# Performance work log

Hardware: AMD Instinct MI355X
Metric: run time of the kernel (lower is better)

Reference implementation:

```python
import jax, jax.numpy as jnp
import numpy as np

N = 50000          # nodes
E_RAND = 800000    # random edges
E = E_RAND + N     # + self loops -> 850000
F_IN = 256         # nembed
F_HID = 64         # nhid
H = 8              # nheads
NCLASS = 40
ALPHA = 0.2        # leakyrelu slope


def setup_inputs() -> dict:
    key = jax.random.key(0)
    ks = jax.random.split(key, 8)
    x = jax.random.normal(ks[0], (N, F_IN), dtype=jnp.float32)
    # random edges + self loops (guarantees every row-sum > 0, like adj + I)
    er = jax.random.randint(ks[1], (2, E_RAND), 0, N, dtype=jnp.int32)
    loops = jnp.tile(jnp.arange(N, dtype=jnp.int32)[None, :], (2, 1))
    edge_index = jnp.concatenate([er, loops], axis=1)  # [2, E]
    # per-head attention params (xavier-ish scale)
    W = jax.random.normal(ks[2], (H, F_IN, F_HID), dtype=jnp.float32) * (1.0 / np.sqrt(F_IN))
    a = jax.random.normal(ks[3], (H, 2 * F_HID), dtype=jnp.float32) * 0.1
    Wo = jax.random.normal(ks[4], (H * F_HID, F_HID), dtype=jnp.float32) * (1.0 / np.sqrt(H * F_HID))
    ao = jax.random.normal(ks[5], (2 * F_HID,), dtype=jnp.float32) * 0.1
    mlp_w = jax.random.normal(ks[6], (NCLASS, F_HID), dtype=jnp.float32) * 0.05
    mlp_b = jnp.zeros((NCLASS,), dtype=jnp.float32)
    return {"x": x, "edge_index": edge_index, "W": W, "a": a,
            "Wo": Wo, "ao": ao, "mlp_w": mlp_w, "mlp_b": mlp_b}


def _leaky(v):
    return jnp.where(v > 0, v, ALPHA * v)


def _spgat_layer(x, W, a, src, dst, n):
    """pyGAT SpGraphAttentionLayer (eval mode, dropout = identity).
    out[i] = sum_{e: src=i} exp(-leakyrelu(a.[h_src;h_dst])) * h[dst] / rowsum_i
    """
    h = x @ W                         # [N, D]
    D = W.shape[1]
    s_src = h @ a[:D]                 # [N]
    s_dst = h @ a[D:]                 # [N]
    # per-edge unnormalized attention (note the -exp(leaky) of original sp impl)
    e = jnp.exp(-_leaky(s_src[src] + s_dst[dst]))          # [E]
    rowsum = jax.ops.segment_sum(e, src, num_segments=n)   # [N]
    num = jax.ops.segment_sum(e[:, None] * h[dst], src, num_segments=n)  # [N, D]
    return num / rowsum[:, None]


def reference(x, edge_index, W, a, Wo, ao, mlp_w, mlp_b):
    src, dst = edge_index[0], edge_index[1]
    # multi-head attention, concat=True -> elu inside each head
    heads = [jax.nn.elu(_spgat_layer(x, W[i], a[i], src, dst, N)) for i in range(H)]
    xc = jnp.concatenate(heads, axis=1)                     # [N, H*F_HID]
    # dropout (eval) = identity
    xo = jax.nn.elu(_spgat_layer(xc, Wo, ao, src, dst, N))  # [N, F_HID]
    return xo @ mlp_w.T + mlp_b                             # [N, NCLASS]
```

## Files before the change

### kernel.cpp

```cpp
#include <hip/hip_runtime.h>

#define NN 50000
#define HH 8
#define ALPHA 0.2f
#define NPAD 50048

typedef short short8 __attribute__((ext_vector_type(8)));
typedef float f32x4 __attribute__((ext_vector_type(4)));

__device__ __forceinline__ float elu_f(float x) {
  return x > 0.f ? x : __expf(x) - 1.f;
}

__device__ __forceinline__ unsigned short f2bf(float f) {
  unsigned int u = __float_as_uint(f);
  unsigned int r = (u + 0x7fffu + ((u >> 16) & 1u)) >> 16;
  return (unsigned short)r;
}

__global__ void cvt_all_kernel(const float* __restrict__ x, unsigned short* __restrict__ xb,
                               const float* __restrict__ W, unsigned short* __restrict__ Wt,
                               const float* __restrict__ Wo, unsigned short* __restrict__ Wot,
                               int n4x) {
  int tid = blockIdx.x * 256 + threadIdx.x;
  if (tid < n4x) {
    float4 v = ((const float4*)x)[tid];
    ushort4 o;
    o.x = f2bf(v.x); o.y = f2bf(v.y); o.z = f2bf(v.z); o.w = f2bf(v.w);
    ((ushort4*)xb)[tid] = o;
    return;
  }
  int t1 = tid - n4x;
  if (t1 < HH * 256 * 64) {
    int h = t1 / (256 * 64);
    int rem = t1 - h * 256 * 64;
    int k = rem >> 6, c = rem & 63;
    Wt[((size_t)h * 64 + c) * 256 + k] = f2bf(W[t1]);
    return;
  }
  int t2 = t1 - HH * 256 * 64;
  if (t2 < 512 * 64) {
    int k = t2 >> 6, c = t2 & 63;
    Wot[(size_t)c * 512 + k] = f2bf(Wo[t2]);
  }
}

__global__ void hist_kernel(const int* __restrict__ src, int* __restrict__ cnt, int E) {
  int e = blockIdx.x * blockDim.x + threadIdx.x;
  if (e < E) atomicAdd(&cnt[src[e]], 1);
}

__global__ __launch_bounds__(1024) void scan_blocks_kernel(const int* __restrict__ cnt,
    int* __restrict__ tmp, int* __restrict__ bsum, int n) {
  __shared__ int sh[1024];
  int i = blockIdx.x * 1024 + threadIdx.x;
  int v = (i < n) ? cnt[i] : 0;
  sh[threadIdx.x] = v;
  __syncthreads();
  for (int off = 1; off < 1024; off <<= 1) {
    int t = (threadIdx.x >= off) ? sh[threadIdx.x - off] : 0;
    __syncthreads();
    sh[threadIdx.x] += t;
    __syncthreads();
  }
  if (i < n) tmp[i] = sh[threadIdx.x] - v;
  if (threadIdx.x == 1023) bsum[blockIdx.x] = sh[1023];
}

__global__ __launch_bounds__(64) void scan_top_kernel(const int* __restrict__ bsum,
    int* __restrict__ boffs, int nb) {
  int L = threadIdx.x;
  int v = (L < nb) ? bsum[L] : 0;
  int incl = v;
#pragma unroll
  for (int off = 1; off < 64; off <<= 1) {
    int t = __shfl_up(incl, off, 64);
    if (L >= off) incl += t;
  }
  if (L < nb) boffs[L] = incl - v;
}

__global__ __launch_bounds__(1024) void scan_apply_kernel(const int* __restrict__ tmp,
    const int* __restrict__ boffs, int* __restrict__ row_ptr, int* __restrict__ nxt,
    int n, int E) {
  int i = blockIdx.x * 1024 + threadIdx.x;
  if (i < n) {
    int s = tmp[i] + boffs[blockIdx.x];
    row_ptr[i] = s;
    nxt[i] = s;
  }
  if (i == 0) row_ptr[n] = E;
}

__global__ void scatter_kernel(const int* __restrict__ src, const int* __restrict__ dst,
                               int* __restrict__ nxt, int* __restrict__ col, int E) {
  int e = blockIdx.x * blockDim.x + threadIdx.x;
  if (e < E) {
    int p = atomicAdd(&nxt[src[e]], 1);
    col[p] = dst[e];
  }
}

__global__ __launch_bounds__(256) void mfma_gemm1_kernel(
    const unsigned short* __restrict__ A, const unsigned short* __restrict__ Bt,
    const float* __restrict__ Aatt, unsigned short* __restrict__ Cout,
    float* __restrict__ ss, float* __restrict__ sd, int N) {
  __shared__ unsigned short Bs[64][264];
  int w = threadIdx.x >> 6, L = threadIdx.x & 63;
  int quad = L >> 4, l16 = L & 15;
  int m0 = blockIdx.x * 64;
  int myrow = m0 + w * 16 + l16;

  const unsigned short* Ar = A + (size_t)myrow * 256 + quad * 8;
  short8 areg[8];
#pragma unroll
  for (int ks = 0; ks < 8; ++ks) areg[ks] = *(const short8*)(Ar + ks * 32);

  for (int y = 0; y < HH; ++y) {
    __syncthreads();
    {
      const unsigned short* Bsrc = Bt + (size_t)y * 64 * 256;
      for (int c = threadIdx.x; c < 2048; c += 256) {
        int n = c >> 5;
        int kq = (c & 31) << 3;
        *(uint4*)&Bs[n][kq] = *(const uint4*)(Bsrc + (size_t)n * 256 + kq);
      }
    }
    __syncthreads();

    f32x4 acc[4];
#pragma unroll
    for (int nt = 0; nt < 4; ++nt) acc[nt] = (f32x4)(0.f);
#pragma unroll
    for (int ks = 0; ks < 8; ++ks) {
#pragma unroll
      for (int nt = 0; nt < 4; ++nt) {
        short8 b = *(const short8*)&Bs[l16 + 16 * nt][ks * 32 + quad * 8];
        acc[nt] = __builtin_amdgcn_mfma_f32_16x16x32_bf16(areg[ks], b, acc[nt], 0, 0, 0);
      }
    }

    float as[4], ad[4];
#pragma unroll
    for (int nt = 0; nt < 4; ++nt) {
      as[nt] = Aatt[y * 128 + l16 + 16 * nt];
      ad[nt] = Aatt[y * 128 + 64 + l16 + 16 * nt];
    }
#pragma unroll
    for (int reg = 0; reg < 4; ++reg) {
      float p = 0.f, q = 0.f;
#pragma unroll
      for (int nt = 0; nt < 4; ++nt) {
        p += acc[nt][reg] * as[nt];
        q += acc[nt][reg] * ad[nt];
      }
#pragma unroll
      for (int off = 1; off < 16; off <<= 1) {
        p += __shfl_xor(p, off, 64);
        q += __shfl_xor(q, off, 64);
      }
      int row = m0 + w * 16 + quad * 4 + reg;
      if (l16 == 0 && row < N) {
        ss[(size_t)row * 8 + y] = p;
        sd[(size_t)row * 8 + y] = q;
      }
    }
#pragma unroll
    for (int reg = 0; reg < 4; ++reg) {
      int row = m0 + w * 16 + quad * 4 + reg;
      if (row < N) {
#pragma unroll
        for (int nt = 0; nt < 4; ++nt)
          Cout[(size_t)row * 512 + y * 64 + l16 + 16 * nt] = f2bf(acc[nt][reg]);
      }
    }
  }
}

__global__ __launch_bounds__(256) void mfma_gemm2_kernel(
    const unsigned short* __restrict__ A, const unsigned short* __restrict__ Bt,
    const float* __restrict__ Aatt, unsigned short* __restrict__ Cout,
    float* __restrict__ ss, float* __restrict__ sd, int N) {
  __shared__ unsigned short Bs[64][520];
  {
    for (int c = threadIdx.x; c < 4096; c += 256) {
      int n = c >> 6;
      int kq = (c & 63) << 3;
      *(uint4*)&Bs[n][kq] = *(const uint4*)(Bt + (size_t)n * 512 + kq);
    }
  }
  __syncthreads();

  int w = threadIdx.x >> 6, L = threadIdx.x & 63;
  int quad = L >> 4, l16 = L & 15;
  int m0 = blockIdx.x * 64;
  int myrow = m0 + w * 16 + l16;
  const unsigned short* Ar = A + (size_t)myrow * 512 + quad * 8;

  f32x4 acc[4];
#pragma unroll
  for (int nt = 0; nt < 4; ++nt) acc[nt] = (f32x4)(0.f);

  short8 a_cur = *(const short8*)(Ar);
  for (int k0 = 0; k0 < 512; k0 += 32) {
    short8 a_nxt;
    if (k0 + 32 < 512) a_nxt = *(const short8*)(Ar + k0 + 32);
#pragma unroll
    for (int nt = 0; nt < 4; ++nt) {
      short8 b = *(const short8*)&Bs[l16 + 16 * nt][k0 + quad * 8];
      acc[nt] = __builtin_amdgcn_mfma_f32_16x16x32_bf16(a_cur, b, acc[nt], 0, 0, 0);
    }
    a_cur = a_nxt;
  }

  float as[4], ad[4];
#pragma unroll
  for (int nt = 0; nt < 4; ++nt) {
    as[nt] = Aatt[l16 + 16 * nt];
    ad[nt] = Aatt[64 + l16 + 16 * nt];
  }
#pragma unroll
  for (int reg = 0; reg < 4; ++reg) {
    float p = 0.f, q = 0.f;
#pragma unroll
    for (int nt = 0; nt < 4; ++nt) {
      p += acc[nt][reg] * as[nt];
      q += acc[nt][reg] * ad[nt];
    }
#pragma unroll
    for (int off = 1; off < 16; off <<= 1) {
      p += __shfl_xor(p, off, 64);
      q += __shfl_xor(q, off, 64);
    }
    int row = m0 + w * 16 + quad * 4 + reg;
    if (l16 == 0 && row < N) { ss[row] = p; sd[row] = q; }
  }
#pragma unroll
  for (int reg = 0; reg < 4; ++reg) {
    int row = m0 + w * 16 + quad * 4 + reg;
    if (row < N) {
#pragma unroll
      for (int nt = 0; nt < 4; ++nt)
        Cout[(size_t)row * 64 + l16 + 16 * nt] = f2bf(acc[nt][reg]);
    }
  }
}

__global__ __launch_bounds__(256) void agg1_kernel(const unsigned short* __restrict__ table,
    const float* __restrict__ ss, const float* __restrict__ sd,
    const int* __restrict__ row_ptr, const int* __restrict__ col,
    unsigned short* __restrict__ xc, int N) {
  int wid = threadIdx.x >> 6, L = threadIdx.x & 63;
  int n = blockIdx.x * 4 + wid;
  if (n >= N) return;
  int h = L >> 3;
  int b = L & 7;
  int srcsel = h << 3;
  float ssn = ss[n * 8 + h];
  int k0 = row_ptr[n], deg = row_ptr[n + 1] - k0;
  float acc[8];
#pragma unroll
  for (int t = 0; t < 8; ++t) acc[t] = 0.f;
  float rs = 0.f;

  for (int c0 = 0; c0 < deg; c0 += 64) {
    int j = c0 + L;
    int d_l = (j < deg) ? col[k0 + j] : 0;
    int m = min(64, deg - c0);
    for (int g = 0; g < m; g += 8) {
      int eoff = g + b;
      int de = __shfl(d_l, eoff, 64);
      float s = ssn + sd[(size_t)de * 8 + h];
      float e = __expf(-fmaxf(s, ALPHA * s));
      if (eoff >= m) e = 0.f;
      rs += e;
      int gm = min(8, m - g);
      uint4 rv[8];
#pragma unroll
      for (int t = 0; t < 8; ++t) {
        if (t < gm) {
          int dg = __builtin_amdgcn_readlane(d_l, g + t);
          rv[t] = *((const uint4*)(table + (size_t)dg * 512) + L);
        }
      }
#pragma unroll
      for (int t = 0; t < 8; ++t) {
        if (t < gm) {
          float ew = __shfl(e, srcsel + t, 64);
          const unsigned int* up = (const unsigned int*)&rv[t];
#pragma unroll
          for (int v = 0; v < 4; ++v) {
            acc[2 * v]     += ew * __uint_as_float(up[v] << 16);
            acc[2 * v + 1] += ew * __uint_as_float(up[v] & 0xffff0000u);
          }
        }
      }
    }
  }
  rs += __shfl_xor(rs, 1, 64);
  rs += __shfl_xor(rs, 2, 64);
  rs += __shfl_xor(rs, 4, 64);
  float inv = 1.f / rs;
  short8 pk;
#pragma unroll
  for (int t = 0; t < 8; ++t) pk[t] = (short)f2bf(elu_f(acc[t] * inv));
  *(short8*)(xc + (size_t)n * 512 + L * 8) = pk;
}

__global__ __launch_bounds__(256) void agg2_kernel(const unsigned short* __restrict__ table,
    const float* __restrict__ ss, const float* __restrict__ sd,
    const int* __restrict__ row_ptr, const int* __restrict__ col,
    float* __restrict__ xo, int N) {
  int wid = threadIdx.x >> 6, L = threadIdx.x & 63;
  int n = blockIdx.x * 4 + wid;
  if (n >= N) return;
  float ssn = ss[n];
  int k0 = row_ptr[n], deg = row_ptr[n + 1] - k0;
  float acc = 0.f, rs = 0.f;
  const char* base = (const char*)table;

  for (int c0 = 0; c0 < deg; c0 += 64) {
    int j = c0 + L;
    int d_l = 0;
    float e_l = 0.f;
    if (j < deg) {
      d_l = col[k0 + j];
      float s = ssn + sd[d_l];
      e_l = __expf(-fmaxf(s, ALPHA * s));
    }
    rs += e_l;
    int m = min(64, deg - c0);
    int off_l = d_l << 7;
    for (int g = 0; g < m; g += 8) {
      int gm = min(8, m - g);
      unsigned hv[8];
#pragma unroll
      for (int t = 0; t < 8; ++t) {
        if (t < gm) {
          int so = __builtin_amdgcn_readlane(off_l, g + t);
          hv[t] = *(const unsigned short*)(base + so + L * 2);
        }
      }
#pragma unroll
      for (int t = 0; t < 8; ++t) {
        if (t < gm) {
          float ew = __uint_as_float(
              (unsigned)__builtin_amdgcn_readlane(__float_as_uint(e_l), g + t));
          acc += ew * __uint_as_float(hv[t] << 16);
        }
      }
    }
  }
#pragma unroll
  for (int off = 1; off < 64; off <<= 1) rs += __shfl_xor(rs, off, 64);
  xo[(size_t)n * 64 + L] = elu_f(acc / rs);
}

__global__ __launch_bounds__(256) void final_kernel(const float* __restrict__ xo,
    const float* __restrict__ mlp_w, const float* __restrict__ mlp_b,
    float* __restrict__ out, int total) {
  __shared__ float wsh[40 * 65];
  __shared__ float bsh[40];
  for (int i = threadIdx.x; i < 40 * 64; i += 256) wsh[(i >> 6) * 65 + (i & 63)] = mlp_w[i];
  if (threadIdx.x < 40) bsh[threadIdx.x] = mlp_b[threadIdx.x];
  __syncthreads();
  int idx = blockIdx.x * 256 + threadIdx.x;
  if (idx >= total) return;
  int n = idx / 40, c = idx - n * 40;
  const float* xr = xo + (size_t)n * 64;
  const float* wr = wsh + c * 65;
  float acc = bsh[c];
#pragma unroll
  for (int j = 0; j < 64; ++j) acc += xr[j] * wr[j];
  out[idx] = acc;
}

extern "C" void kernel_launch(void* const* d_in, const int* in_sizes, int n_in,
                              void* d_out, int out_size, void* d_ws, size_t ws_size,
                              hipStream_t stream) {
  (void)n_in; (void)out_size; (void)ws_size;
  const float* x  = (const float*)d_in[0];
  const int*   ei = (const int*)d_in[1];
  const float* W  = (const float*)d_in[2];
  const float* a  = (const float*)d_in[3];
  const float* Wo = (const float*)d_in[4];
  const float* ao = (const float*)d_in[5];
  const float* mw = (const float*)d_in[6];
  const float* mb = (const float*)d_in[7];
  float* out = (float*)d_out;

  const int N = NN;
  const int E = in_sizes[1] / 2;
  const int* src = ei;
  const int* dst = ei + E;

  char* ws = (char*)d_ws;
  size_t off = 0;
  auto alloc = [&](size_t bytes) {
    char* p = ws + off;
    off = (off + bytes + 255) & ~(size_t)255;
    return p;
  };
  unsigned short* xb  = (unsigned short*)alloc((size_t)NPAD * 256 * 2);
  unsigned short* Wt  = (unsigned short*)alloc((size_t)HH * 64 * 256 * 2);
  unsigned short* Wot = (unsigned short*)alloc((size_t)64 * 512 * 2);
  unsigned short* h1b = (unsigned short*)alloc((size_t)N * 512 * 2);
  float* ss1     = (float*)alloc((size_t)N * 8 * 4);
  float* sd1     = (float*)alloc((size_t)N * 8 * 4);
  unsigned short* xc = (unsigned short*)alloc((size_t)NPAD * 512 * 2);
  unsigned short* h2b = (unsigned short*)alloc((size_t)N * 64 * 2);
  float* ss2     = (float*)alloc((size_t)N * 4);
  float* sd2     = (float*)alloc((size_t)N * 4);
  float* xo      = (float*)alloc((size_t)N * 64 * 4);
  int*   row_ptr = (int*)  alloc((size_t)(N + 1) * 4);
  int*   nxt     = (int*)  alloc((size_t)N * 4);
  int*   cnt     = (int*)  alloc((size_t)N * 4);
  int*   tmp     = (int*)  alloc((size_t)N * 4);
  int*   bsum    = (int*)  alloc(64 * 4);
  int*   boffs   = (int*)  alloc(64 * 4);
  int*   colv    = (int*)  alloc((size_t)E * 4);

  int eb = (E + 255) / 256;
  int nb1024 = (N + 1023) / 1024;
  int n4x = N * 256 / 4;
  int cvt_total = n4x + HH * 256 * 64 + 512 * 64;

  hipLaunchKernelGGL(cvt_all_kernel, dim3((cvt_total + 255) / 256), dim3(256), 0, stream,
                     x, xb, W, Wt, Wo, Wot, n4x);

  hipMemsetAsync(cnt, 0, (size_t)N * 4, stream);
  hipLaunchKernelGGL(hist_kernel, dim3(eb), dim3(256), 0, stream, src, cnt, E);
  hipLaunchKernelGGL(scan_blocks_kernel, dim3(nb1024), dim3(1024), 0, stream, cnt, tmp, bsum, N);
  hipLaunchKernelGGL(scan_top_kernel, dim3(1), dim3(64), 0, stream, bsum, boffs, nb1024);
  hipLaunchKernelGGL(scan_apply_kernel, dim3(nb1024), dim3(1024), 0, stream, tmp, boffs, row_ptr, nxt, N, E);
  hipLaunchKernelGGL(scatter_kernel, dim3(eb), dim3(256), 0, stream, src, dst, nxt, colv, E);

  hipLaunchKernelGGL(mfma_gemm1_kernel, dim3(NPAD / 64), dim3(256), 0, stream,
                     xb, Wt, a, h1b, ss1, sd1, N);
  hipLaunchKernelGGL(agg1_kernel, dim3((N + 3) / 4), dim3(256), 0, stream,
                     h1b, ss1, sd1, row_ptr, colv, xc, N);

  hipLaunchKernelGGL(mfma_gemm2_kernel, dim3(NPAD / 64), dim3(256), 0, stream,
                     xc, Wot, ao, h2b, ss2, sd2, N);
  hipLaunchKernelGGL(agg2_kernel, dim3((N + 3) / 4), dim3(256), 0, stream,
                     h2b, ss2, sd2, row_ptr, colv, xo, N);

  hipLaunchKernelGGL(final_kernel, dim3((N * 40 + 255) / 256), dim3(256), 0, stream,
                     xo, mw, mb, out, N * 40);
}
```

Baseline: 457.2 us.

## Fuse x bf16 conversion into GEMM1, fuse final MLP into agg2, dst-sort CSR

Drops the separate fp32-to-bf16 pass over x and converts rows on load inside the first MFMA GEMM. Fuses the output MLP into the second aggregation kernel through shared memory, so the xo intermediate is never written or reread. Rebuilds the CSR by first bucketing edges by destination, then scattering by source, so each row's column list comes out roughly sorted by dst and neighbour gathers are more local. The cost is extra histogram, scan and scatter work plus an eid buffer.

Measured after the change: 525.7 us. 15.0% more time.

```diff
diff --git a/kernel.cpp b/kernel.cpp
--- a/kernel.cpp
+++ b/kernel.cpp
@@ -18,43 +18,38 @@
   return (unsigned short)r;
 }
 
-__global__ void cvt_all_kernel(const float* __restrict__ x, unsigned short* __restrict__ xb,
-                               const float* __restrict__ W, unsigned short* __restrict__ Wt,
-                               const float* __restrict__ Wo, unsigned short* __restrict__ Wot,
-                               int n4x) {
+__global__ void cvt_w_kernel(const float* __restrict__ W, unsigned short* __restrict__ Wt,
+                             const float* __restrict__ Wo, unsigned short* __restrict__ Wot) {
   int tid = blockIdx.x * 256 + threadIdx.x;
-  if (tid < n4x) {
-    float4 v = ((const float4*)x)[tid];
-    ushort4 o;
-    o.x = f2bf(v.x); o.y = f2bf(v.y); o.z = f2bf(v.z); o.w = f2bf(v.w);
-    ((ushort4*)xb)[tid] = o;
+  if (tid < HH * 256 * 64) {
+    int h = tid / (256 * 64);
+    int rem = tid - h * 256 * 64;
+    int k = rem >> 6, c = rem & 63;
+    Wt[((size_t)h * 64 + c) * 256 + k] = f2bf(W[tid]);
     return;
   }
-  int t1 = tid - n4x;
-  if (t1 < HH * 256 * 64) {
-    int h = t1 / (256 * 64);
-    int rem = t1 - h * 256 * 64;
-    int k = rem >> 6, c = rem & 63;
-    Wt[((size_t)h * 64 + c) * 256 + k] = f2bf(W[t1]);
-    return;
-  }
-  int t2 = t1 - HH * 256 * 64;
+  int t2 = tid - HH * 256 * 64;
   if (t2 < 512 * 64) {
     int k = t2 >> 6, c = t2 & 63;
     Wot[(size_t)c * 512 + k] = f2bf(Wo[t2]);
   }
 }
 
-__global__ void hist_kernel(const int* __restrict__ src, int* __restrict__ cnt, int E) {
+__global__ void hist_both_kernel(const int* __restrict__ src, const int* __restrict__ dst,
+                                 int* __restrict__ cnt2, int N, int E) {
   int e = blockIdx.x * blockDim.x + threadIdx.x;
-  if (e < E) atomicAdd(&cnt[src[e]], 1);
-}
-
-__global__ __launch_bounds__(1024) void scan_blocks_kernel(const int* __restrict__ cnt,
-    int* __restrict__ tmp, int* __restrict__ bsum, int n) {
+  if (e < E) {
+    atomicAdd(&cnt2[src[e]], 1);
+    atomicAdd(&cnt2[N + dst[e]], 1);
+  }
+}
+
+__global__ __launch_bounds__(1024) void scan_blocks2_kernel(const int* __restrict__ cnt2,
+    int* __restrict__ tmp2, int* __restrict__ bsum2, int n) {
   __shared__ int sh[1024];
+  int y = blockIdx.y;
   int i = blockIdx.x * 1024 + threadIdx.x;
-  int v = (i < n) ? cnt[i] : 0;
+  int v = (i < n) ? cnt2[(size_t)y * n + i] : 0;
   sh[threadIdx.x] = v;
   __syncthreads();
   for (int off = 1; off < 1024; off <<= 1) {
@@ -63,46 +58,58 @@
     sh[threadIdx.x] += t;
     __syncthreads();
   }
-  if (i < n) tmp[i] = sh[threadIdx.x] - v;
-  if (threadIdx.x == 1023) bsum[blockIdx.x] = sh[1023];
-}
-
-__global__ __launch_bounds__(64) void scan_top_kernel(const int* __restrict__ bsum,
-    int* __restrict__ boffs, int nb) {
-  int L = threadIdx.x;
-  int v = (L < nb) ? bsum[L] : 0;
+  if (i < n) tmp2[(size_t)y * n + i] = sh[threadIdx.x] - v;
+  if (threadIdx.x == 1023) bsum2[y * 64 + blockIdx.x] = sh[1023];
+}
+
+__global__ __launch_bounds__(128) void scan_top2_kernel(const int* __restrict__ bsum2,
+    int* __restrict__ boffs2, int nb) {
+  int y = threadIdx.x >> 6, L = threadIdx.x & 63;
+  int v = (L < nb) ? bsum2[y * 64 + L] : 0;
   int incl = v;
 #pragma unroll
   for (int off = 1; off < 64; off <<= 1) {
     int t = __shfl_up(incl, off, 64);
     if (L >= off) incl += t;
   }
-  if (L < nb) boffs[L] = incl - v;
-}
-
-__global__ __launch_bounds__(1024) void scan_apply_kernel(const int* __restrict__ tmp,
-    const int* __restrict__ boffs, int* __restrict__ row_ptr, int* __restrict__ nxt,
-    int n, int E) {
+  if (L < nb) boffs2[y * 64 + L] = incl - v;
+}
+
+__global__ __launch_bounds__(1024) void scan_apply2_kernel(const int* __restrict__ tmp2,
+    const int* __restrict__ boffs2, int* __restrict__ row_ptr, int* __restrict__ nxt,
+    int* __restrict__ nxtd, int n, int E) {
+  int y = blockIdx.y;
   int i = blockIdx.x * 1024 + threadIdx.x;
   if (i < n) {
-    int s = tmp[i] + boffs[blockIdx.x];
-    row_ptr[i] = s;
-    nxt[i] = s;
-  }
-  if (i == 0) row_ptr[n] = E;
-}
-
-__global__ void scatter_kernel(const int* __restrict__ src, const int* __restrict__ dst,
-                               int* __restrict__ nxt, int* __restrict__ col, int E) {
+    int s = tmp2[(size_t)y * n + i] + boffs2[y * 64 + blockIdx.x];
+    if (y == 0) { row_ptr[i] = s; nxt[i] = s; }
+    else nxtd[i] = s;
+  }
+  if (i == 0 && y == 0) row_ptr[n] = E;
+}
+
+__global__ void scatter_d_kernel(const int* __restrict__ dst, int* __restrict__ nxtd,
+                                 int* __restrict__ eid, int E) {
   int e = blockIdx.x * blockDim.x + threadIdx.x;
   if (e < E) {
+    int p = atomicAdd(&nxtd[dst[e]], 1);
+    eid[p] = e;
+  }
+}
+
+__global__ void scatter_s_kernel(const int* __restrict__ src, const int* __restrict__ dst,
+                                 const int* __restrict__ eid, int* __restrict__ nxt,
+                                 int* __restrict__ col, int E) {
+  int k = blockIdx.x * blockDim.x + threadIdx.x;
+  if (k < E) {
+    int e = eid[k];
     int p = atomicAdd(&nxt[src[e]], 1);
     col[p] = dst[e];
   }
 }
 
 __global__ __launch_bounds__(256) void mfma_gemm1_kernel(
-    const unsigned short* __restrict__ A, const unsigned short* __restrict__ Bt,
+    const float* __restrict__ X, const unsigned short* __restrict__ Bt,
     const float* __restrict__ Aatt, unsigned short* __restrict__ Cout,
     float* __restrict__ ss, float* __restrict__ sd, int N) {
   __shared__ unsigned short Bs[64][264];
@@ -110,11 +117,19 @@
   int quad = L >> 4, l16 = L & 15;
   int m0 = blockIdx.x * 64;
   int myrow = m0 + w * 16 + l16;
-
-  const unsigned short* Ar = A + (size_t)myrow * 256 + quad * 8;
+  int rowc = min(myrow, N - 1);
+
+  const float* Ar = X + (size_t)rowc * 256 + quad * 8;
   short8 areg[8];
 #pragma unroll
-  for (int ks = 0; ks < 8; ++ks) areg[ks] = *(const short8*)(Ar + ks * 32);
+  for (int ks = 0; ks < 8; ++ks) {
+    float4 a0 = *(const float4*)(Ar + ks * 32);
+    float4 a1 = *(const float4*)(Ar + ks * 32 + 4);
+    areg[ks][0] = (short)f2bf(a0.x); areg[ks][1] = (short)f2bf(a0.y);
+    areg[ks][2] = (short)f2bf(a0.z); areg[ks][3] = (short)f2bf(a0.w);
+    areg[ks][4] = (short)f2bf(a1.x); areg[ks][5] = (short)f2bf(a1.y);
+    areg[ks][6] = (short)f2bf(a1.z); areg[ks][7] = (short)f2bf(a1.w);
+  }
 
   for (int y = 0; y < HH; ++y) {
     __syncthreads();
@@ -307,72 +322,73 @@
   *(short8*)(xc + (size_t)n * 512 + L * 8) = pk;
 }
 
-__global__ __launch_bounds__(256) void agg2_kernel(const unsigned short* __restrict__ table,
+__global__ __launch_bounds__(256) void agg2_final_kernel(const unsigned short* __restrict__ table,
     const float* __restrict__ ss, const float* __restrict__ sd,
     const int* __restrict__ row_ptr, const int* __restrict__ col,
-    float* __restrict__ xo, int N) {
-  int wid = threadIdx.x >> 6, L = threadIdx.x & 63;
-  int n = blockIdx.x * 4 + wid;
-  if (n >= N) return;
-  float ssn = ss[n];
-  int k0 = row_ptr[n], deg = row_ptr[n + 1] - k0;
-  float acc = 0.f, rs = 0.f;
-  const char* base = (const char*)table;
-
-  for (int c0 = 0; c0 < deg; c0 += 64) {
-    int j = c0 + L;
-    int d_l = 0;
-    float e_l = 0.f;
-    if (j < deg) {
-      d_l = col[k0 + j];
-      float s = ssn + sd[d_l];
-      e_l = __expf(-fmaxf(s, ALPHA * s));
-    }
-    rs += e_l;
-    int m = min(64, deg - c0);
-    int off_l = d_l << 7;
-    for (int g = 0; g < m; g += 8) {
-      int gm = min(8, m - g);
-      unsigned hv[8];
-#pragma unroll
-      for (int t = 0; t < 8; ++t) {
-        if (t < gm) {
-          int so = __builtin_amdgcn_readlane(off_l, g + t);
-          hv[t] = *(const unsigned short*)(base + so + L * 2);
-        }
-      }
-#pragma unroll
-      for (int t = 0; t < 8; ++t) {
-        if (t < gm) {
-          float ew = __uint_as_float(
-              (unsigned)__builtin_amdgcn_readlane(__float_as_uint(e_l), g + t));
-          acc += ew * __uint_as_float(hv[t] << 16);
-        }
-      }
-    }
-  }
-#pragma unroll
-  for (int off = 1; off < 64; off <<= 1) rs += __shfl_xor(rs, off, 64);
-  xo[(size_t)n * 64 + L] = elu_f(acc / rs);
-}
-
-__global__ __launch_bounds__(256) void final_kernel(const float* __restrict__ xo,
     const float* __restrict__ mlp_w, const float* __restrict__ mlp_b,
-    float* __restrict__ out, int total) {
+    float* __restrict__ out, int N) {
   __shared__ float wsh[40 * 65];
   __shared__ float bsh[40];
+  __shared__ float osh[4][68];
   for (int i = threadIdx.x; i < 40 * 64; i += 256) wsh[(i >> 6) * 65 + (i & 63)] = mlp_w[i];
   if (threadIdx.x < 40) bsh[threadIdx.x] = mlp_b[threadIdx.x];
   __syncthreads();
-  int idx = blockIdx.x * 256 + threadIdx.x;
-  if (idx >= total) return;
-  int n = idx / 40, c = idx - n * 40;
-  const float* xr = xo + (size_t)n * 64;
-  const float* wr = wsh + c * 65;
-  float acc = bsh[c];
-#pragma unroll
-  for (int j = 0; j < 64; ++j) acc += xr[j] * wr[j];
-  out[idx] = acc;
+
+  int wid = threadIdx.x >> 6, L = threadIdx.x & 63;
+  int n = blockIdx.x * 4 + wid;
+  bool act = (n < N);
+  float o = 0.f;
+  if (act) {
+    float ssn = ss[n];
+    int k0 = row_ptr[n], deg = row_ptr[n + 1] - k0;
+    float acc = 0.f, rs = 0.f;
+    const char* base = (const char*)table;
+    for (int c0 = 0; c0 < deg; c0 += 64) {
+      int j = c0 + L;
+      int d_l = 0;
+      float e_l = 0.f;
+      if (j < deg) {
+        d_l = col[k0 + j];
+        float s = ssn + sd[d_l];
+        e_l = __expf(-fmaxf(s, ALPHA * s));
+      }
+      rs += e_l;
+      int m = min(64, deg - c0);
+      int off_l = d_l << 7;
+      for (int g = 0; g < m; g += 8) {
+        int gm = min(8, m - g);
+        unsigned hv[8];
+#pragma unroll
+        for (int t = 0; t < 8; ++t) {
+          if (t < gm) {
+            int so = __builtin_amdgcn_readlane(off_l, g + t);
+            hv[t] = *(const unsigned short*)(base + so + L * 2);
+          }
+        }
+#pragma unroll
+        for (int t = 0; t < 8; ++t) {
+          if (t < gm) {
+            float ew = __uint_as_float(
+                (unsigned)__builtin_amdgcn_readlane(__float_as_uint(e_l), g + t));
+            acc += ew * __uint_as_float(hv[t] << 16);
+          }
+        }
+      }
+    }
+#pragma unroll
+    for (int off = 1; off < 64; off <<= 1) rs += __shfl_xor(rs, off, 64);
+    o = elu_f(acc / rs);
+  }
+  osh[wid][L] = o;
+  __syncthreads();
+  if (act && L < 40) {
+    const float* wr = wsh + L * 65;
+    const float* orow = osh[wid];
+    float acc = bsh[L];
+#pragma unroll
+    for (int j = 0; j < 64; ++j) acc += orow[j] * wr[j];
+    out[(size_t)n * 40 + L] = acc;
+  }
 }
 
 extern "C" void kernel_launch(void* const* d_in, const int* in_sizes, int n_in,
@@ -401,7 +417,6 @@
     off = (off + bytes + 255) & ~(size_t)255;
     return p;
   };
-  unsigned short* xb  = (unsigned short*)alloc((size_t)NPAD * 256 * 2);
   unsigned short* Wt  = (unsigned short*)alloc((size_t)HH * 64 * 256 * 2);
   unsigned short* Wot = (unsigned short*)alloc((size_t)64 * 512 * 2);
   unsigned short* h1b = (unsigned short*)alloc((size_t)N * 512 * 2);
@@ -411,40 +426,38 @@
   unsigned short* h2b = (unsigned short*)alloc((size_t)N * 64 * 2);
   float* ss2     = (float*)alloc((size_t)N * 4);
   float* sd2     = (float*)alloc((size_t)N * 4);
-  float* xo      = (float*)alloc((size_t)N * 64 * 4);
   int*   row_ptr = (int*)  alloc((size_t)(N + 1) * 4);
   int*   nxt     = (int*)  alloc((size_t)N * 4);
-  int*   cnt     = (int*)  alloc((size_t)N * 4);
-  int*   tmp     = (int*)  alloc((size_t)N * 4);
-  int*   bsum    = (int*)  alloc(64 * 4);
-  int*   boffs   = (int*)  alloc(64 * 4);
+  int*   nxtd    = (int*)  alloc((size_t)N * 4);
+  int*   cnt2    = (int*)  alloc((size_t)2 * N * 4);
+  int*   tmp2    = (int*)  alloc((size_t)2 * N * 4);
+  int*   bsum2   = (int*)  alloc(128 * 4);
+  int*   boffs2  = (int*)  alloc(128 * 4);
+  int*   eid     = (int*)  alloc((size_t)E * 4);
   int*   colv    = (int*)  alloc((size_t)E * 4);
 
   int eb = (E + 255) / 256;
   int nb1024 = (N + 1023) / 1024;
-  int n4x = N * 256 / 4;
-  int cvt_total = n4x + HH * 256 * 64 + 512 * 64;
-
-  hipLaunchKernelGGL(cvt_all_kernel, dim3((cvt_total + 255) / 256), dim3(256), 0, stream,
-                     x, xb, W, Wt, Wo, Wot, n4x);
-
-  hipMemsetAsync(cnt, 0, (size_t)N * 4, stream);
-  hipLaunchKernelGGL(hist_kernel, dim3(eb), dim3(256), 0, stream, src, cnt, E);
-  hipLaunchKernelGGL(scan_blocks_kernel, dim3(nb1024), dim3(1024), 0, stream, cnt, tmp, bsum, N);
-  hipLaunchKernelGGL(scan_top_kernel, dim3(1), dim3(64), 0, stream, bsum, boffs, nb1024);
-  hipLaunchKernelGGL(scan_apply_kernel, dim3(nb1024), dim3(1024), 0, stream, tmp, boffs, row_ptr, nxt, N, E);
-  hipLaunchKernelGGL(scatter_kernel, dim3(eb), dim3(256), 0, stream, src, dst, nxt, colv, E);
+
+  hipLaunchKernelGGL(cvt_w_kernel, dim3((HH * 256 * 64 + 512 * 64 + 255) / 256), dim3(256),
+                     0, stream, W, Wt, Wo, Wot);
+
+  hipMemsetAsync(cnt2, 0, (size_t)2 * N * 4, stream);
+  hipLaunchKernelGGL(hist_both_kernel, dim3(eb), dim3(256), 0, stream, src, dst, cnt2, N, E);
+  hipLaunchKernelGGL(scan_blocks2_kernel, dim3(nb1024, 2), dim3(1024), 0, stream, cnt2, tmp2, bsum2, N);
+  hipLaunchKernelGGL(scan_top2_kernel, dim3(1), dim3(128), 0, stream, bsum2, boffs2, nb1024);
+  hipLaunchKernelGGL(scan_apply2_kernel, dim3(nb1024, 2), dim3(1024), 0, stream,
+                     tmp2, boffs2, row_ptr, nxt, nxtd, N, E);
+  hipLaunchKernelGGL(scatter_d_kernel, dim3(eb), dim3(256), 0, stream, dst, nxtd, eid, E);
+  hipLaunchKernelGGL(scatter_s_kernel, dim3(eb), dim3(256), 0, stream, src, dst, eid, nxt, colv, E);
 
   hipLaunchKernelGGL(mfma_gemm1_kernel, dim3(NPAD / 64), dim3(256), 0, stream,
-                     xb, Wt, a, h1b, ss1, sd1, N);
+                     x, Wt, a, h1b, ss1, sd1, N);
   hipLaunchKernelGGL(agg1_kernel, dim3((N + 3) / 4), dim3(256), 0, stream,
                      h1b, ss1, sd1, row_ptr, colv, xc, N);
 
   hipLaunchKernelGGL(mfma_gemm2_kernel, dim3(NPAD / 64), dim3(256), 0, stream,
                      xc, Wot, ao, h2b, ss2, sd2, N);
-  hipLaunchKernelGGL(agg2_kernel, dim3((N + 3) / 4), dim3(256), 0, stream,
-                     h2b, ss2, sd2, row_ptr, colv, xo, N);
-
-  hipLaunchKernelGGL(final_kernel, dim3((N * 40 + 255) / 256), dim3(256), 0, stream,
-                     xo, mw, mb, out, N * 40);
-}
+  hipLaunchKernelGGL(agg2_final_kernel, dim3((N + 3) / 4), dim3(256), 0, stream,
+                     h2b, ss2, sd2, row_ptr, colv, mw, mb, out, N);
+}
```
